# Performance work log

Measured on AMD Instinct MI355X. Metric: run time of the kernel, lower is better.

## Reference

```python
import jax, jax.numpy as jnp
import numpy as np

# Loss hyperparameters (from init_kwargs defaults)
ALPHA, BETA, GAMMA = 1.0, 2.0, 1.0
DAY_W, NIGHT_W = 2.0, 0.5
PEAK_WIN_W, PEAK_WIN = 3.0, 2
HIGH_POWER_W, POWER_PCT = 1.5, 0.75
HOURS = 24

B, S = 4096, 4032  # seq_len = 24 * 168 days


def setup_inputs() -> dict:
    key = jax.random.key(0)
    k1, k2 = jax.random.split(key)
    y_true = jax.random.uniform(k1, (B, S), dtype=jnp.float32)
    # predictions = truth + noise, clipped to be realistic power values
    y_pred = y_true + 0.1 * jax.random.normal(k2, (B, S), dtype=jnp.float32)
    return {"y_pred": y_pred, "y_true": y_true}


def _daily_peaks(y, day_mask):
    # y, day_mask: (B, D, H). Peaks restricted to daytime hours.
    masked = jnp.where(day_mask, y, jnp.float32(-1e9))
    times = jnp.argmax(masked, axis=-1)                                   # (B, D) int
    vals = jnp.take_along_axis(y, times[..., None], axis=-1)[..., 0]      # (B, D)
    return times, vals


def reference(y_pred, y_true):
    b, s = y_true.shape
    d = s // HOURS
    # default is_daytime: hour-of-day in [6, 20]
    hour = jnp.arange(HOURS, dtype=jnp.int32)
    day_hour_mask = (hour >= 6) & (hour <= 20)                            # (H,)
    is_daytime = jnp.broadcast_to(day_hour_mask[None, None, :], (b, d, HOURS))

    yt = y_true.reshape(b, d, HOURS)
    yp = y_pred.reshape(b, d, HOURS)

    true_times, true_peaks = _daily_peaks(yt, is_daytime)
    pred_times, pred_peaks = _daily_peaks(yp, is_daytime)
    peak_time_errors = (pred_times - true_times).astype(jnp.float32)      # (B, D)

    # --- step weights: day/night base, x PEAK_WIN_W in [peak-2, peak+2] ---
    base_w = jnp.where(is_daytime, jnp.float32(DAY_W), jnp.float32(NIGHT_W))  # (B,D,H)
    pt = true_times[..., None]                                            # (B,D,1)
    in_window = (hour[None, None, :] >= pt - PEAK_WIN) & (hour[None, None, :] <= pt + PEAK_WIN)
    step_w = base_w * jnp.where(in_window, jnp.float32(PEAK_WIN_W), jnp.float32(1.0))
    step_w = step_w.reshape(b, s)

    sq_err = (y_pred - y_true) ** 2
    L_overall = jnp.sum(sq_err * step_w) / jnp.sum(step_w)

    # --- peak magnitude loss with high-power sample weighting ---
    sample_avg_peaks = jnp.mean(true_peaks, axis=1)                       # (B,)
    thr = jnp.quantile(sample_avg_peaks, POWER_PCT)
    high = sample_avg_peaks > thr                                         # (B,) bool
    sample_w = jnp.where(high[:, None], jnp.float32(HIGH_POWER_W), jnp.float32(1.0))
    sample_w = jnp.broadcast_to(sample_w, true_peaks.shape)               # (B, D)
    peak_sq = (pred_peaks - true_peaks) ** 2
    L_peak_mag = jnp.sum(peak_sq * sample_w) / jnp.sum(sample_w)

    L_peak_timing = jnp.mean(jnp.abs(peak_time_errors) * 10.0)

    return ALPHA * L_overall + BETA * L_peak_mag + GAMMA * L_peak_timing
```

## Files before the change

### kernel.cpp

```cpp
#include <hip/hip_runtime.h>
#include <math.h>

#define S_LEN   4032
#define HOURS   24
#define DAYS    168
#define DAY_PAD 28
#define NB_MAX  4096


__device__ inline float block_reduce_f(float v, float* scratch, int tid) {
#pragma unroll
    for (int o = 32; o > 0; o >>= 1) v += __shfl_down(v, o, 64);
    if ((tid & 63) == 0) scratch[tid >> 6] = v;
    __syncthreads();
    float r = 0.f;
    if (tid == 0) r = scratch[0] + scratch[1] + scratch[2] + scratch[3];
    __syncthreads();
    return r;
}

__device__ inline double block_reduce_d(double v, double* scratch, int tid) {
#pragma unroll
    for (int o = 32; o > 0; o >>= 1) v += __shfl_down(v, o, 64);
    if ((tid & 63) == 0) scratch[tid >> 6] = v;
    __syncthreads();
    double r = 0.0;
    if (tid == 0) r = scratch[0] + scratch[1] + scratch[2] + scratch[3];
    __syncthreads();
    return r;
}


__global__ __launch_bounds__(256, 4) void day_kernel(
    const float* __restrict__ y_pred, const float* __restrict__ y_true,
    float* __restrict__ A, float* __restrict__ P,
    float* __restrict__ SEp, float* __restrict__ SWp, float* __restrict__ Tp)
{
    __shared__ float s_yt[DAYS * DAY_PAD];
    __shared__ float s_yp[DAYS * DAY_PAD];
    __shared__ float s_red[4];

    const int tid = threadIdx.x;
    const int b = blockIdx.x;
    const size_t base = (size_t)b * S_LEN;
    const float4* gp = (const float4*)(y_pred + base);
    const float4* gt = (const float4*)(y_true + base);

    for (int i = tid; i < S_LEN / 4; i += 256) {
        float4 vp = gp[i];
        float4 vt = gt[i];
        int f = i * 4;
        int d = f / HOURS;
        int off = f - d * HOURS;
        *(float4*)&s_yp[d * DAY_PAD + off] = vp;
        *(float4*)&s_yt[d * DAY_PAD + off] = vt;
    }
    __syncthreads();

    float tpeak = 0.f, psq = 0.f, se = 0.f, sw = 0.f, terr = 0.f;
    if (tid < DAYS) {
        const float4* rt = (const float4*)&s_yt[tid * DAY_PAD];
        const float4* rp = (const float4*)&s_yp[tid * DAY_PAD];
        float yt[HOURS];
#pragma unroll
        for (int j = 0; j < 6; ++j) {
            float4 q = rt[j];
            yt[j * 4 + 0] = q.x; yt[j * 4 + 1] = q.y;
            yt[j * 4 + 2] = q.z; yt[j * 4 + 3] = q.w;
        }
        float tbest = yt[6]; int tt = 6;
#pragma unroll
        for (int h = 7; h <= 20; ++h) {
            if (yt[h] > tbest) { tbest = yt[h]; tt = h; }
        }
        float pbest = -1e30f; int pt = 6;
#pragma unroll
        for (int j = 0; j < 6; ++j) {
            float4 q = rp[j];
            float pv[4] = {q.x, q.y, q.z, q.w};
#pragma unroll
            for (int k = 0; k < 4; ++k) {
                int h = j * 4 + k;
                float v = pv[k];
                bool day = (h >= 6) && (h <= 20);
                if (day && v > pbest) { pbest = v; pt = h; }
                float bw = day ? 2.0f : 0.5f;
                float w = bw * (((h >= tt - 2) && (h <= tt + 2)) ? 3.0f : 1.0f);
                float dd = v - yt[h];
                se += dd * dd * w;
                sw += w;
            }
        }
        tpeak = tbest;
        float dp = pbest - tbest;
        psq = dp * dp;
        terr = fabsf((float)(pt - tt));
    }

    float rA = block_reduce_f(tpeak, s_red, tid);
    float rP = block_reduce_f(psq,   s_red, tid);
    float rE = block_reduce_f(se,    s_red, tid);
    float rW = block_reduce_f(sw,    s_red, tid);
    float rT = block_reduce_f(terr,  s_red, tid);
    if (tid == 0) {
        A[b]   = rA * (1.0f / (float)DAYS);
        P[b]   = rP;
        SEp[b] = rE;
        SWp[b] = rW;
        Tp[b]  = rT;
    }
}


__global__ __launch_bounds__(256) void finalize_kernel(
    const float* __restrict__ A, const float* __restrict__ P,
    const float* __restrict__ SEp, const float* __restrict__ SWp,
    const float* __restrict__ Tp, float* __restrict__ out, int nB)
{
    __shared__ unsigned s_keys[NB_MAX];
    __shared__ unsigned s_hist[256];
    __shared__ unsigned s_wtot[4];
    __shared__ unsigned s_sel, s_srem;
    __shared__ double s_dred[4];

    const int tid = threadIdx.x;

    for (int i = tid; i < nB; i += 256) {
        unsigned u = __float_as_uint(A[i]);
        s_keys[i] = (u & 0x80000000u) ? ~u : (u | 0x80000000u);
    }
    __syncthreads();

    double pos = 0.75 * (double)(nB - 1);
    int lo = (int)pos;
    double frac = pos - (double)lo;
    int hi = (lo + 1 < nB) ? lo + 1 : lo;
    int ranks[2] = {lo, hi};
    float qv[2];

    for (int sidx = 0; sidx < 2; ++sidx) {
        int rem = ranks[sidx];
        unsigned prefix = 0;
        for (int shift = 24; shift >= 0; shift -= 8) {
            s_hist[tid] = 0;
            __syncthreads();
            unsigned maskAbove = (shift == 24) ? 0u : (0xFFFFFFFFu << (shift + 8));
            for (int i = tid; i < nB; i += 256) {
                unsigned k = s_keys[i];
                if ((k & maskAbove) == prefix)
                    atomicAdd(&s_hist[(k >> shift) & 0xFFu], 1u);
            }
            __syncthreads();
            unsigned c = s_hist[tid];
            unsigned x = c;
#pragma unroll
            for (int o = 1; o < 64; o <<= 1) {
                unsigned y = __shfl_up(x, o, 64);
                if ((tid & 63) >= o) x += y;
            }
            if ((tid & 63) == 63) s_wtot[tid >> 6] = x;
            __syncthreads();
            unsigned woff = 0;
            for (int w2 = 0; w2 < (tid >> 6); ++w2) woff += s_wtot[w2];
            unsigned incl = woff + x;
            unsigned excl = incl - c;
            if ((unsigned)rem >= excl && (unsigned)rem < incl) {
                s_sel = (unsigned)tid;
                s_srem = (unsigned)rem - excl;
            }
            __syncthreads();
            prefix |= (s_sel << shift);
            rem = (int)s_srem;
            __syncthreads();
        }
        unsigned bits = (prefix & 0x80000000u) ? (prefix & 0x7FFFFFFFu) : ~prefix;
        qv[sidx] = __uint_as_float(bits);
    }

    float thr = (float)((double)qv[0] + frac * ((double)qv[1] - (double)qv[0]));

    double wp = 0.0, wsum = 0.0, se = 0.0, swt = 0.0, te = 0.0;
    for (int i = tid; i < nB; i += 256) {
        float a = A[i];
        float w = (a > thr) ? 1.5f : 1.0f;
        wp   += (double)w * (double)P[i];
        wsum += (double)w;
        se   += (double)SEp[i];
        swt  += (double)SWp[i];
        te   += (double)Tp[i];
    }
    wp   = block_reduce_d(wp,   s_dred, tid);
    wsum = block_reduce_d(wsum, s_dred, tid);
    se   = block_reduce_d(se,   s_dred, tid);
    swt  = block_reduce_d(swt,  s_dred, tid);
    te   = block_reduce_d(te,   s_dred, tid);

    if (tid == 0) {
        double L_overall = se / swt;
        double L_peak    = wp / ((double)DAYS * wsum);
        double L_timing  = 10.0 * te / ((double)nB * (double)DAYS);
        out[0] = (float)(L_overall + 2.0 * L_peak + L_timing);
    }
}


extern "C" void kernel_launch(void* const* d_in, const int* in_sizes, int n_in,
                              void* d_out, int out_size, void* d_ws, size_t ws_size,
                              hipStream_t stream) {
    const float* y_pred = (const float*)d_in[0];
    const float* y_true = (const float*)d_in[1];
    int total = in_sizes[0];
    int nB = total / S_LEN;

    float* ws  = (float*)d_ws;
    float* A   = ws;
    float* P   = ws + 1 * NB_MAX;
    float* SEp = ws + 2 * NB_MAX;
    float* SWp = ws + 3 * NB_MAX;
    float* Tp  = ws + 4 * NB_MAX;

    day_kernel<<<nB, 256, 0, stream>>>(y_pred, y_true, A, P, SEp, SWp, Tp);
    finalize_kernel<<<1, 256, 0, stream>>>(A, P, SEp, SWp, Tp, (float*)d_out, nB);
}
```

Before: 175.9 us.

## Map one wavefront per 64 days with direct global loads, drop LDS staging

The day kernel now assigns each 64-lane wavefront a slice of 64 days of one sample, and each lane loads its own day straight from global memory into registers instead of staging the whole row in shared memory. Per-wave partial sums replace the block reductions and their barriers. The finalize kernel combines the three partials per sample, and the radix-select histogram uses ballot-based peer aggregation to cut LDS atomics. Each lane's 96-byte strided loads may coalesce worse than the old contiguous float4 sweep, and a quarter of the lanes in the third wave per sample sit idle.

```diff
diff --git a/kernel.cpp b/kernel.cpp
--- a/kernel.cpp
+++ b/kernel.cpp
@@ -4,20 +4,82 @@
 #define S_LEN   4032
 #define HOURS   24
 #define DAYS    168
-#define DAY_PAD 28
-#define NB_MAX  4096
-
-
-__device__ inline float block_reduce_f(float v, float* scratch, int tid) {
-#pragma unroll
-    for (int o = 32; o > 0; o >>= 1) v += __shfl_down(v, o, 64);
-    if ((tid & 63) == 0) scratch[tid >> 6] = v;
-    __syncthreads();
-    float r = 0.f;
-    if (tid == 0) r = scratch[0] + scratch[1] + scratch[2] + scratch[3];
-    __syncthreads();
-    return r;
-}
+#define WPS     3
+
+
+__global__ __launch_bounds__(256) void day_kernel(
+    const float* __restrict__ y_pred, const float* __restrict__ y_true,
+    float* __restrict__ Apart, float* __restrict__ Ppart,
+    float* __restrict__ SEpart, float* __restrict__ SWpart, float* __restrict__ Tpart,
+    int nW)
+{
+    const int lane = threadIdx.x & 63;
+    const int w = blockIdx.x * 4 + (threadIdx.x >> 6);
+    if (w >= nW) return;
+    const int b = w / WPS;
+    const int part = w - b * WPS;
+    const int day = part * 64 + lane;
+    const bool active = day < DAYS;
+    const int dc = active ? day : (DAYS - 1);
+
+    const float4* gt = (const float4*)(y_true + (size_t)b * S_LEN + (size_t)dc * HOURS);
+    const float4* gp = (const float4*)(y_pred + (size_t)b * S_LEN + (size_t)dc * HOURS);
+
+    float yt[24], yp[24];
+    {
+        float4 t0 = gt[0], t1 = gt[1], t2 = gt[2], t3 = gt[3], t4 = gt[4], t5 = gt[5];
+        float4 p0 = gp[0], p1 = gp[1], p2 = gp[2], p3 = gp[3], p4 = gp[4], p5 = gp[5];
+        yt[0]=t0.x; yt[1]=t0.y; yt[2]=t0.z; yt[3]=t0.w;
+        yt[4]=t1.x; yt[5]=t1.y; yt[6]=t1.z; yt[7]=t1.w;
+        yt[8]=t2.x; yt[9]=t2.y; yt[10]=t2.z; yt[11]=t2.w;
+        yt[12]=t3.x; yt[13]=t3.y; yt[14]=t3.z; yt[15]=t3.w;
+        yt[16]=t4.x; yt[17]=t4.y; yt[18]=t4.z; yt[19]=t4.w;
+        yt[20]=t5.x; yt[21]=t5.y; yt[22]=t5.z; yt[23]=t5.w;
+        yp[0]=p0.x; yp[1]=p0.y; yp[2]=p0.z; yp[3]=p0.w;
+        yp[4]=p1.x; yp[5]=p1.y; yp[6]=p1.z; yp[7]=p1.w;
+        yp[8]=p2.x; yp[9]=p2.y; yp[10]=p2.z; yp[11]=p2.w;
+        yp[12]=p3.x; yp[13]=p3.y; yp[14]=p3.z; yp[15]=p3.w;
+        yp[16]=p4.x; yp[17]=p4.y; yp[18]=p4.z; yp[19]=p4.w;
+        yp[20]=p5.x; yp[21]=p5.y; yp[22]=p5.z; yp[23]=p5.w;
+    }
+
+    float tbest = yt[6]; int tt = 6;
+#pragma unroll
+    for (int h = 7; h <= 20; ++h) if (yt[h] > tbest) { tbest = yt[h]; tt = h; }
+    float pbest = yp[6]; int pt = 6;
+#pragma unroll
+    for (int h = 7; h <= 20; ++h) if (yp[h] > pbest) { pbest = yp[h]; pt = h; }
+
+    float se = 0.f, sw = 0.f;
+#pragma unroll
+    for (int h = 0; h < 24; ++h) {
+        const bool dayh = (h >= 6) && (h <= 20);
+        const float bw = dayh ? 2.0f : 0.5f;
+        float wg = bw * (((h >= tt - 2) && (h <= tt + 2)) ? 3.0f : 1.0f);
+        float d = yp[h] - yt[h];
+        se = fmaf(d * d, wg, se);
+        sw += wg;
+    }
+
+    float tpeak = tbest;
+    float dp = pbest - tbest;
+    float psq = dp * dp;
+    float terr = fabsf((float)(pt - tt));
+    if (!active) { tpeak = 0.f; psq = 0.f; se = 0.f; sw = 0.f; terr = 0.f; }
+
+#pragma unroll
+    for (int o = 32; o > 0; o >>= 1) {
+        tpeak += __shfl_down(tpeak, o, 64);
+        psq   += __shfl_down(psq,   o, 64);
+        se    += __shfl_down(se,    o, 64);
+        sw    += __shfl_down(sw,    o, 64);
+        terr  += __shfl_down(terr,  o, 64);
+    }
+    if (lane == 0) {
+        Apart[w] = tpeak; Ppart[w] = psq; SEpart[w] = se; SWpart[w] = sw; Tpart[w] = terr;
+    }
+}
+
 
 __device__ inline double block_reduce_d(double v, double* scratch, int tid) {
 #pragma unroll
@@ -30,92 +92,12 @@
     return r;
 }
 
-
-__global__ __launch_bounds__(256, 4) void day_kernel(
-    const float* __restrict__ y_pred, const float* __restrict__ y_true,
-    float* __restrict__ A, float* __restrict__ P,
-    float* __restrict__ SEp, float* __restrict__ SWp, float* __restrict__ Tp)
-{
-    __shared__ float s_yt[DAYS * DAY_PAD];
-    __shared__ float s_yp[DAYS * DAY_PAD];
-    __shared__ float s_red[4];
-
-    const int tid = threadIdx.x;
-    const int b = blockIdx.x;
-    const size_t base = (size_t)b * S_LEN;
-    const float4* gp = (const float4*)(y_pred + base);
-    const float4* gt = (const float4*)(y_true + base);
-
-    for (int i = tid; i < S_LEN / 4; i += 256) {
-        float4 vp = gp[i];
-        float4 vt = gt[i];
-        int f = i * 4;
-        int d = f / HOURS;
-        int off = f - d * HOURS;
-        *(float4*)&s_yp[d * DAY_PAD + off] = vp;
-        *(float4*)&s_yt[d * DAY_PAD + off] = vt;
-    }
-    __syncthreads();
-
-    float tpeak = 0.f, psq = 0.f, se = 0.f, sw = 0.f, terr = 0.f;
-    if (tid < DAYS) {
-        const float4* rt = (const float4*)&s_yt[tid * DAY_PAD];
-        const float4* rp = (const float4*)&s_yp[tid * DAY_PAD];
-        float yt[HOURS];
-#pragma unroll
-        for (int j = 0; j < 6; ++j) {
-            float4 q = rt[j];
-            yt[j * 4 + 0] = q.x; yt[j * 4 + 1] = q.y;
-            yt[j * 4 + 2] = q.z; yt[j * 4 + 3] = q.w;
-        }
-        float tbest = yt[6]; int tt = 6;
-#pragma unroll
-        for (int h = 7; h <= 20; ++h) {
-            if (yt[h] > tbest) { tbest = yt[h]; tt = h; }
-        }
-        float pbest = -1e30f; int pt = 6;
-#pragma unroll
-        for (int j = 0; j < 6; ++j) {
-            float4 q = rp[j];
-            float pv[4] = {q.x, q.y, q.z, q.w};
-#pragma unroll
-            for (int k = 0; k < 4; ++k) {
-                int h = j * 4 + k;
-                float v = pv[k];
-                bool day = (h >= 6) && (h <= 20);
-                if (day && v > pbest) { pbest = v; pt = h; }
-                float bw = day ? 2.0f : 0.5f;
-                float w = bw * (((h >= tt - 2) && (h <= tt + 2)) ? 3.0f : 1.0f);
-                float dd = v - yt[h];
-                se += dd * dd * w;
-                sw += w;
-            }
-        }
-        tpeak = tbest;
-        float dp = pbest - tbest;
-        psq = dp * dp;
-        terr = fabsf((float)(pt - tt));
-    }
-
-    float rA = block_reduce_f(tpeak, s_red, tid);
-    float rP = block_reduce_f(psq,   s_red, tid);
-    float rE = block_reduce_f(se,    s_red, tid);
-    float rW = block_reduce_f(sw,    s_red, tid);
-    float rT = block_reduce_f(terr,  s_red, tid);
-    if (tid == 0) {
-        A[b]   = rA * (1.0f / (float)DAYS);
-        P[b]   = rP;
-        SEp[b] = rE;
-        SWp[b] = rW;
-        Tp[b]  = rT;
-    }
-}
-
+#define NB_MAX 4096
 
 __global__ __launch_bounds__(256) void finalize_kernel(
-    const float* __restrict__ A, const float* __restrict__ P,
-    const float* __restrict__ SEp, const float* __restrict__ SWp,
-    const float* __restrict__ Tp, float* __restrict__ out, int nB)
+    const float* __restrict__ Apart, const float* __restrict__ Ppart,
+    const float* __restrict__ SEpart, const float* __restrict__ SWpart,
+    const float* __restrict__ Tpart, float* __restrict__ out, int nB, int nW)
 {
     __shared__ unsigned s_keys[NB_MAX];
     __shared__ unsigned s_hist[256];
@@ -124,9 +106,11 @@
     __shared__ double s_dred[4];
 
     const int tid = threadIdx.x;
+    const int lane = tid & 63;
 
     for (int i = tid; i < nB; i += 256) {
-        unsigned u = __float_as_uint(A[i]);
+        float a = (Apart[3 * i] + Apart[3 * i + 1] + Apart[3 * i + 2]) * (1.0f / (float)DAYS);
+        unsigned u = __float_as_uint(a);
         s_keys[i] = (u & 0x80000000u) ? ~u : (u | 0x80000000u);
     }
     __syncthreads();
@@ -134,8 +118,7 @@
     double pos = 0.75 * (double)(nB - 1);
     int lo = (int)pos;
     double frac = pos - (double)lo;
-    int hi = (lo + 1 < nB) ? lo + 1 : lo;
-    int ranks[2] = {lo, hi};
+    int ranks[2] = {lo, (lo + 1 < nB) ? lo + 1 : lo};
     float qv[2];
 
     for (int sidx = 0; sidx < 2; ++sidx) {
@@ -147,8 +130,20 @@
             unsigned maskAbove = (shift == 24) ? 0u : (0xFFFFFFFFu << (shift + 8));
             for (int i = tid; i < nB; i += 256) {
                 unsigned k = s_keys[i];
-                if ((k & maskAbove) == prefix)
-                    atomicAdd(&s_hist[(k >> shift) & 0xFFu], 1u);
+                bool act = ((k & maskAbove) == prefix);
+                unsigned digit = (k >> shift) & 0xFFu;
+                unsigned long long peers = __ballot(act);
+#pragma unroll
+                for (int bit = 0; bit < 8; ++bit) {
+                    bool mine = (digit >> bit) & 1u;
+                    unsigned long long vote = __ballot(act && mine);
+                    peers &= mine ? vote : ~vote;
+                }
+                if (act) {
+                    int leader = __ffsll((unsigned long long)peers) - 1;
+                    if (lane == leader)
+                        atomicAdd(&s_hist[digit], (unsigned)__popcll(peers));
+                }
             }
             __syncthreads();
             unsigned c = s_hist[tid];
@@ -178,16 +173,20 @@
     }
 
     float thr = (float)((double)qv[0] + frac * ((double)qv[1] - (double)qv[0]));
+    unsigned tu = __float_as_uint(thr);
+    unsigned thrKey = (tu & 0x80000000u) ? ~tu : (tu | 0x80000000u);
 
     double wp = 0.0, wsum = 0.0, se = 0.0, swt = 0.0, te = 0.0;
     for (int i = tid; i < nB; i += 256) {
-        float a = A[i];
-        float w = (a > thr) ? 1.5f : 1.0f;
-        wp   += (double)w * (double)P[i];
+        float w = (s_keys[i] > thrKey) ? 1.5f : 1.0f;
+        float Pb = Ppart[3 * i] + Ppart[3 * i + 1] + Ppart[3 * i + 2];
+        wp   += (double)w * (double)Pb;
         wsum += (double)w;
-        se   += (double)SEp[i];
-        swt  += (double)SWp[i];
-        te   += (double)Tp[i];
+    }
+    for (int i = tid; i < nW; i += 256) {
+        se  += (double)SEpart[i];
+        swt += (double)SWpart[i];
+        te  += (double)Tpart[i];
     }
     wp   = block_reduce_d(wp,   s_dred, tid);
     wsum = block_reduce_d(wsum, s_dred, tid);
@@ -211,14 +210,16 @@
     const float* y_true = (const float*)d_in[1];
     int total = in_sizes[0];
     int nB = total / S_LEN;
-
-    float* ws  = (float*)d_ws;
-    float* A   = ws;
-    float* P   = ws + 1 * NB_MAX;
-    float* SEp = ws + 2 * NB_MAX;
-    float* SWp = ws + 3 * NB_MAX;
-    float* Tp  = ws + 4 * NB_MAX;
-
-    day_kernel<<<nB, 256, 0, stream>>>(y_pred, y_true, A, P, SEp, SWp, Tp);
-    finalize_kernel<<<1, 256, 0, stream>>>(A, P, SEp, SWp, Tp, (float*)d_out, nB);
-}
+    int nW = nB * WPS;
+
+    float* ws    = (float*)d_ws;
+    float* Apart = ws;
+    float* Ppart = ws + 1 * (size_t)nW;
+    float* SEp   = ws + 2 * (size_t)nW;
+    float* SWp   = ws + 3 * (size_t)nW;
+    float* Tp    = ws + 4 * (size_t)nW;
+
+    int nBlocks = (nW + 3) / 4;
+    day_kernel<<<nBlocks, 256, 0, stream>>>(y_pred, y_true, Apart, Ppart, SEp, SWp, Tp, nW);
+    finalize_kernel<<<1, 256, 0, stream>>>(Apart, Ppart, SEp, SWp, Tp, (float*)d_out, nB, nW);
+}
```

New measurement: 210.5 us. 19.7% more time.
